# Performance work log

Measured on AMD Instinct MI355X. Metric: run time of the kernel, lower is better.

## Reference

```python
import jax, jax.numpy as jnp
from jax import lax
import numpy as np

RATIO = 4
CNT = 2  # sz=5 -> sz//2 in fineshift
B, C, H, W = 4, 8, 1024, 1024
K = 9

# --- half-pixel interpolation kernels (precomputed exactly as in fineshift) ---
_HALF = np.asarray([0.5, 0.305334091185, 0, -0.072698593239, 0, 0.021809577942,
                    0, -0.005192756653, 0, 0.000807762146, 0, -6.0081482e-05]) * 2.0
_FULL23 = np.concatenate([_HALF[1:][::-1], _HALF])   # 23-tap symmetric interp kernel
_DEC12 = _FULL23[::2]                                 # kernel[..., ::2] decimation -> 12 taps
K_S = np.concatenate([_DEC12, [0.0]])[:, None]        # 'S': (13,1), zero row appended
K_E = np.concatenate([_DEC12, [0.0]])[None, :]        # 'E': (1,13), zero col appended
K_SE = np.zeros((13, 13))
K_SE[:12, :12] = np.outer(_DEC12, _DEC12)             # 'SE': separable xy kernel + zero row/col


def _depthwise_same(x, k2d):
    # depthwise conv, identical kernel per band, torch padding='same' semantics
    c = x.shape[1]
    kh, kw = k2d.shape
    k = jnp.broadcast_to(jnp.asarray(k2d, x.dtype), (c, 1, kh, kw))
    pad = ((kh // 2, kh - 1 - kh // 2), (kw // 2, kw - 1 - kw // 2))
    return lax.conv_general_dilated(x, k, (1, 1), pad, feature_group_count=c)


def setup_inputs() -> dict:
    key = jax.random.key(0)
    k1, k2, k3, k4 = jax.random.split(key, 4)
    outputs = jax.random.normal(k1, (B, C, H, W), jnp.float32)
    mtf = jax.random.normal(k2, (K, K, C), jnp.float32) * 0.1
    r = jax.random.randint(k3, (B, C), 0, 5, jnp.int32)
    c = jax.random.randint(k4, (B, C), 0, 5, jnp.int32)
    return {"outputs": outputs, "mtf": mtf, "r": r, "c": c}


def reference(outputs, mtf, r, c):
    nb = outputs.shape[1]
    ksz = mtf.shape[0]
    pad = (ksz - 1) // 2
    # ReplicationPad2d + valid depthwise MTF blur (== pad + conv in original)
    xp = jnp.pad(outputs, ((0, 0), (0, 0), (pad, pad), (pad, pad)), mode='edge')
    w = jnp.transpose(mtf, (2, 0, 1))[:, None].astype(outputs.dtype)  # (C,1,K,K)
    x = lax.conv_general_dilated(xp, w, (1, 1), 'VALID', feature_group_count=nb)

    # --- fineshift, vectorized over batch and band (replaces per-batch loop + boolean masks) ---
    r_int, c_int = r // 2, c // 2
    r_frac, c_frac = r % 2, c % 2
    x_S = _depthwise_same(x, K_S)
    x_E = _depthwise_same(x, K_E)
    x_SE = _depthwise_same(x, K_SE)
    m = lambda cond: cond[:, :, None, None]
    x = jnp.where(m((r_frac == 1) & (c_frac == 1)), x_SE,
        jnp.where(m((r_frac == 1) & (c_frac == 0)), x_S,
        jnp.where(m((r_frac == 0) & (c_frac == 1)), x_E, x)))

    # integer shift: one-hot 5x5 'same' conv == out[y,x] = img[y - r_int, x - c_int], zeros outside
    hh, ww = x.shape[-2], x.shape[-1]
    def shift_one(img, ri, ci):
        p = jnp.pad(img, CNT)
        return lax.dynamic_slice(p, (CNT - ri, CNT - ci), (hh, ww))
    x = jax.vmap(jax.vmap(shift_one))(x, r_int, c_int)

    if RATIO == 2:
        return x[:, :, 1::RATIO, 1::RATIO]
    return x[:, :, 2::RATIO, 2::RATIO]
```

## Files before the change

kernel.cpp:

```cpp
#include <hip/hip_runtime.h>

typedef _Float16 half2v __attribute__((ext_vector_type(2)));
typedef _Float16 half4v __attribute__((ext_vector_type(4)));
typedef _Float16 half8v __attribute__((ext_vector_type(8)));

#define HH 1024
#define OHW 256
#define TH 16
#define TW 32
#define NR 80
#define NCH 18
#define ROWH 160
#define NTHREADS 256
#define ESPAN 528

#define NMAIN 4096
#define NEDGE 384
#define NCORN 288
#define NAUX  (NEDGE + NCORN)

#if defined(__has_builtin)
#  if __has_builtin(__builtin_amdgcn_fdot2)
#    define HAS_FDOT2 1
#  endif
#endif
#ifndef HAS_FDOT2
#  define HAS_FDOT2 0
#endif

__constant__ float DEC12c[12] = {
  -1.20162964e-04f,  1.615524292e-03f, -1.0385513306e-02f,  4.3619155884e-02f,
  -1.45397186478e-01f, 6.10668182370e-01f, 6.10668182370e-01f, -1.45397186478e-01f,
   4.3619155884e-02f, -1.0385513306e-02f,  1.615524292e-03f, -1.20162964e-04f
};

__device__ __forceinline__ int clampi(int v) { return v < 0 ? 0 : (v > HH - 1 ? HH - 1 : v); }

__device__ __forceinline__ int swzc(int c, int r) {
  return c ^ ((c >> 3) & 1) ^ ((r >> 2) & 3);
}

__device__ __forceinline__ half2v mk2(_Float16 a, _Float16 b) {
  half2v r; r.x = a; r.y = b; return r;
}

template<int J>
__device__ __forceinline__ half2v sel3(half8v a, half8v b, half8v c) {
  constexpr int V = J >> 2, E = J & 3;
  const half8v s = (V == 0) ? a : (V == 1) ? b : c;
  return mk2(s[2 * E], s[2 * E + 1]);
}
template<int E>
__device__ __forceinline__ half2v g2(half8v v) { return mk2(v[2 * E], v[2 * E + 1]); }

__device__ __forceinline__ float dot2acc(half2v w, half2v k, float acc) {
#if HAS_FDOT2
  return __builtin_amdgcn_fdot2(w, k, acc, false);
#else
  return acc + (float)w.x * (float)k.x + (float)w.y * (float)k.y;
#endif
}

__global__ __launch_bounds__(128) void dgp_ckbuild(
    const float* __restrict__ mtfp, const int* __restrict__ rp,
    const int* __restrict__ cp, _Float16* __restrict__ ckg) {
  __shared__ float kva[180];
  __shared__ float mlds[81];
  __shared__ float avs[12], bvs[12];
  const int tid = threadIdx.x;
  const int bz = blockIdx.x;
  const int chC = bz & 7;
  const int rv = rp[bz], cv = cp[bz];
  const int rf = rv & 1, cf = cv & 1;

  if (tid < 12)       avs[tid] = rf ? DEC12c[tid] : (tid == 6 ? 1.f : 0.f);
  else if (tid < 24)  bvs[tid - 12] = cf ? DEC12c[tid - 12] : (tid - 12 == 6 ? 1.f : 0.f);
  else if (tid < 105) { const int m = tid - 24; mlds[m] = mtfp[m * 8 + chC]; }
  __syncthreads();

  for (int i = tid; i < 180; i += 128) {
    const int S = i / 9, v = i - S * 9;
    const int plo = (S - 8 > 0) ? S - 8 : 0, phi = (S < 11) ? S : 11;
    float s1 = 0.f;
    for (int p = plo; p <= phi; ++p) s1 += avs[p] * mlds[(S - p) * 9 + v];
    kva[i] = s1;
  }
  __syncthreads();

  half2v* out2 = (half2v*)ckg;
  for (int i = tid; i < 200; i += 128) {
    const int S = i / 10, m = i - S * 10;
    float s[2];
    #pragma unroll
    for (int h = 0; h < 2; ++h) {
      const int T = 2 * m + h;
      const int qlo = (T - 8 > 0) ? T - 8 : 0, qhi = (T < 11) ? T : 11;
      float acc = 0.f;
      for (int q = qlo; q <= qhi; ++q) acc += bvs[q] * kva[S * 9 + (T - q)];
      s[h] = acc;
    }
    out2[bz * 320 + S * 16 + m] = mk2((_Float16)s[0], (_Float16)s[1]);
  }
}

__global__ __launch_bounds__(NTHREADS) void dgp_fused(
    const float* __restrict__ inp, const float* __restrict__ mtfp,
    const int* __restrict__ rp, const int* __restrict__ cp,
    const _Float16* __restrict__ ckg, float* __restrict__ outg,
    float* __restrict__ dumpf) {
  __shared__ __align__(64) unsigned char smem[25600];
  const int tid = threadIdx.x;
  const int b = blockIdx.x;

  if (b >= NAUX) {
    _Float16* tile = (_Float16*)smem;
    const int bm = b - NAUX;
    const int bxt = bm & 7, by = (bm >> 3) & 15, bz = bm >> 7;
    const int rv = rp[bz], cv = cp[bz];
    const int ri = rv >> 1, ci = cv >> 1;
    const int R0 = 4 * TH * by - 8 - ri;
    const int C0 = 4 * TW * bxt - 8 - ci;

    const float* src = inp + ((size_t)bz << 20);
    for (int idx = tid; idx < NR * NCH; idx += NTHREADS) {
      const int rr = idx / 18, g = idx - 18 * rr;
      const float* grow = src + (clampi(R0 + rr) << 10);
      const int c0 = C0 + 8 * g;
      float v[8];
      if (c0 >= 0 && c0 + 7 <= HH - 1) {
        __builtin_memcpy(v, grow + c0, 32);
      } else {
        #pragma unroll
        for (int i = 0; i < 8; ++i) v[i] = grow[clampi(c0 + i)];
      }
      _Float16 h[8];
      #pragma unroll
      for (int i = 0; i < 8; ++i) h[i] = (_Float16)v[i];
      __builtin_memcpy(tile + rr * ROWH + (swzc(g, rr) << 3), h, 16);
    }
    __syncthreads();

    const int ty = tid >> 4;
    const int tx = tid & 15;
    const int rbase = 4 * ty;
    const size_t kbase = (size_t)bz * 640;

    float a0e = 0.f, a0o = 0.f, a1e = 0.f, a1o = 0.f;

#define DOT_STEP(s_) do {                                                \
    const int r_ = rbase + (s_);                                         \
    const _Float16* rp_ = tile + r_ * ROWH;                              \
    const half8v w0 = *(const half8v*)(rp_ + (swzc(tx + 0, r_) << 3));   \
    const half8v w1 = *(const half8v*)(rp_ + (swzc(tx + 1, r_) << 3));   \
    const half8v w2 = *(const half8v*)(rp_ + (swzc(tx + 2, r_) << 3));   \
    const _Float16* kp_ = ckg + kbase + (s_) * 32;                       \
    const half8v K0 = *(const half8v*)(kp_);                             \
    const half8v K1 = *(const half8v*)(kp_ + 8);                         \
    const half4v K2 = *(const half4v*)(kp_ + 16);                        \
    a0e = dot2acc(sel3<0>(w0, w1, w2), g2<0>(K0), a0e);                  \
    a0o = dot2acc(sel3<1>(w0, w1, w2), g2<1>(K0), a0o);                  \
    a0e = dot2acc(sel3<2>(w0, w1, w2), g2<2>(K0), a0e);                  \
    a0o = dot2acc(sel3<3>(w0, w1, w2), g2<3>(K0), a0o);                  \
    a0e = dot2acc(sel3<4>(w0, w1, w2), g2<0>(K1), a0e);                  \
    a0o = dot2acc(sel3<5>(w0, w1, w2), g2<1>(K1), a0o);                  \
    a0e = dot2acc(sel3<6>(w0, w1, w2), g2<2>(K1), a0e);                  \
    a0o = dot2acc(sel3<7>(w0, w1, w2), g2<3>(K1), a0o);                  \
    a0e = dot2acc(sel3<8>(w0, w1, w2), mk2(K2[0], K2[1]), a0e);          \
    a0o = dot2acc(sel3<9>(w0, w1, w2), mk2(K2[2], K2[3]), a0o);          \
    a1e = dot2acc(sel3<2>(w0, w1, w2), g2<0>(K0), a1e);                  \
    a1o = dot2acc(sel3<3>(w0, w1, w2), g2<1>(K0), a1o);                  \
    a1e = dot2acc(sel3<4>(w0, w1, w2), g2<2>(K0), a1e);                  \
    a1o = dot2acc(sel3<5>(w0, w1, w2), g2<3>(K0), a1o);                  \
    a1e = dot2acc(sel3<6>(w0, w1, w2), g2<0>(K1), a1e);                  \
    a1o = dot2acc(sel3<7>(w0, w1, w2), g2<1>(K1), a1o);                  \
    a1e = dot2acc(sel3<8>(w0, w1, w2), g2<2>(K1), a1e);                  \
    a1o = dot2acc(sel3<9>(w0, w1, w2), g2<3>(K1), a1o);                  \
    a1e = dot2acc(sel3<10>(w0, w1, w2), mk2(K2[0], K2[1]), a1e);         \
    a1o = dot2acc(sel3<11>(w0, w1, w2), mk2(K2[2], K2[3]), a1o);         \
  } while (0)

    DOT_STEP(0);  DOT_STEP(1);  DOT_STEP(2);  DOT_STEP(3);  DOT_STEP(4);
    DOT_STEP(5);  DOT_STEP(6);  DOT_STEP(7);  DOT_STEP(8);  DOT_STEP(9);
    DOT_STEP(10); DOT_STEP(11); DOT_STEP(12); DOT_STEP(13); DOT_STEP(14);
    DOT_STEP(15); DOT_STEP(16); DOT_STEP(17); DOT_STEP(18); DOT_STEP(19);
#undef DOT_STEP

    const int oi = TH * by + ty;
    const int oj0 = TW * bxt + 2 * tx;
    const int oj1 = oj0 + 1;
    float* orow = outg + ((size_t)bz * OHW + oi) * OHW + oj0;
    float* dump = dumpf + tid;
    const bool rowbad = (oi < 2) | (oi == 255);
    float* d0 = (rowbad | (oj0 < 2) | (oj0 == 255)) ? dump : orow;
    float* d1 = (rowbad | (oj1 < 2) | (oj1 == 255)) ? dump : (orow + 1);
    *d0 = a0e + a0o;
    *d1 = a1e + a1o;
  } else if (b < NEDGE) {
    _Float16* tileh = (_Float16*)smem;
    float* ck   = (float*)(smem + 21120);
    float* kva  = (float*)(smem + 22720);
    float* mlds = (float*)(smem + 23440);
    float* avs  = (float*)(smem + 23764);
    float* bvs  = (float*)(smem + 23812);

    const int e = b;
    const int bx = e & 1;
    const int t = e >> 1;
    const int segi6 = t % 6;
    const int bz = t / 6;
    const bool isRow = (segi6 < 3);
    const int segi = isRow ? segi6 : segi6 - 3;
    const int fixedo = (segi == 2) ? 255 : segi;
    const int chC = bz & 7;
    const int rv = rp[bz], cv = cp[bz];
    const int ri = rv >> 1, rf = rv & 1, ci = cv >> 1, cf = cv & 1;

    if (tid < 12) {
      float av = rf ? DEC12c[tid] : (tid == 6 ? 1.f : 0.f);
      if (isRow) {
        const int xi = (2 + 4 * fixedo - ri) - 6 + tid;
        if (xi < 0 || xi >= HH) av = 0.f;
      }
      avs[tid] = av;
    } else if (tid < 24) {
      const int q = tid - 12;
      float bv = cf ? DEC12c[q] : (q == 6 ? 1.f : 0.f);
      if (!isRow) {
        const int xj = (2 + 4 * fixedo - ci) - 6 + q;
        if (xj < 0 || xj >= HH) bv = 0.f;
      }
      bvs[q] = bv;
    } else if (tid < 105) {
      const int m = tid - 24; mlds[m] = mtfp[m * 8 + chC];
    }
    __syncthreads();

    for (int i = tid; i < 180; i += NTHREADS) {
      const int S = i / 9, v = i - S * 9;
      const int plo = (S - 8 > 0) ? S - 8 : 0, phi = (S < 11) ? S : 11;
      float s1 = 0.f;
      for (int p = plo; p <= phi; ++p) s1 += avs[p] * mlds[(S - p) * 9 + v];
      kva[i] = s1;
    }
    __syncthreads();
    for (int i = tid; i < 400; i += NTHREADS) {
      const int S = i / 20, T = i - S * 20;
      const int qlo = (T - 8 > 0) ? T - 8 : 0, qhi = (T < 11) ? T : 11;
      float s1 = 0.f;
      for (int q = qlo; q <= qhi; ++q) s1 += bvs[q] * kva[S * 9 + (T - q)];
      ck[i] = s1;
    }

    const float* src = inp + ((size_t)bz << 20);
    if (isRow) {
      const int R0e = (2 + 4 * fixedo - ri) - 10;
      const int C0c = 512 * bx - 8 - ci;
      for (int i = tid; i < 20 * 66; i += NTHREADS) {
        const int rr = i / 66, jc = i - rr * 66;
        const float* grow = src + (clampi(R0e + rr) << 10);
        const int c0 = C0c + 8 * jc;
        float v[8];
        if (c0 >= 0 && c0 + 7 <= HH - 1) {
          __builtin_memcpy(v, grow + c0, 32);
        } else {
          #pragma unroll
          for (int k = 0; k < 8; ++k) v[k] = grow[clampi(c0 + k)];
        }
        _Float16 h[8];
        #pragma unroll
        for (int k = 0; k < 8; ++k) h[k] = (_Float16)v[k];
        __builtin_memcpy(tileh + rr * ESPAN + 8 * jc, h, 16);
      }
    } else {
      const int Cw0 = (2 + 4 * fixedo - ci) - 10;
      const int Rr0 = 512 * bx - 8 - ri;
      for (int i = tid; i < 20 * ESPAN; i += NTHREADS) {
        const int rr = i / 20, T = i - rr * 20;
        tileh[T * ESPAN + rr] =
            (_Float16)src[(clampi(Rr0 + rr) << 10) + clampi(Cw0 + T)];
      }
    }
    __syncthreads();

    if (tid < 128) {
      float acc = 0.f;
      for (int L = 0; L < 20; ++L) {
        const _Float16* wp = tileh + L * ESPAN + 4 * tid;
        #pragma unroll
        for (int j = 0; j < 5; ++j) {
          half4v h4;
          __builtin_memcpy(&h4, wp + 4 * j, 8);
          #pragma unroll
          for (int k = 0; k < 4; ++k) {
            const int ee = 4 * j + k;
            const float cv2 = isRow ? ck[L * 20 + ee] : ck[ee * 20 + L];
            acc += cv2 * (float)h4[k];
          }
        }
      }
      int oi, oj;
      if (isRow) { oi = fixedo; oj = 128 * bx + tid; }
      else       { oj = fixedo; oi = 128 * bx + tid; }
      const int ov = isRow ? oj : oi;
      if (ov != 0 && ov != 1 && ov != 255)
        outg[((size_t)bz * OHW + oi) * OHW + oj] = acc;
    }
  } else {
    float* mlds = (float*)smem;
    float* avs  = (float*)(smem + 324);
    float* bvs  = (float*)(smem + 372);

    const int c = b - NEDGE;
    const int bi = c % 3;
    const int t = c / 3;
    const int bj = t % 3;
    const int bz = t / 3;
    const int oi = (bi == 2) ? 255 : bi;
    const int oj = (bj == 2) ? 255 : bj;
    const int chC = bz & 7;
    const int rv = rp[bz], cv = cp[bz];
    const int ri = rv >> 1, rf = rv & 1, ci = cv >> 1, cf = cv & 1;

    if (tid < 12)       avs[tid] = rf ? DEC12c[tid] : (tid == 6 ? 1.f : 0.f);
    else if (tid < 24)  bvs[tid - 12] = cf ? DEC12c[tid - 12] : (tid - 12 == 6 ? 1.f : 0.f);
    if (tid < 81) mlds[tid] = mtfp[tid * 8 + chC];
    __syncthreads();
    if (tid >= 64) return;

    const int Ri = 2 + 4 * oi - ri;
    const int Cj = 2 + 4 * oj - ci;
    const float* src = inp + ((size_t)bz << 20);

    float acc = 0.f;
    for (int pair = tid; pair < 144; pair += 64) {
      const int p = pair / 12, q = pair - 12 * (pair / 12);
      const int xi = Ri - 6 + p, xj = Cj - 6 + q;
      if (xi < 0 || xi >= HH || xj < 0 || xj >= HH) continue;
      const float ab = avs[p] * bvs[q];
      if (ab == 0.f) continue;
      float s = 0.f;
      #pragma unroll
      for (int u = 0; u < 9; ++u) {
        const float* grow = src + (clampi(xi - 4 + u) << 10);
        #pragma unroll
        for (int v = 0; v < 9; ++v) s += mlds[u * 9 + v] * grow[clampi(xj - 4 + v)];
      }
      acc += ab * s;
    }
    #pragma unroll
    for (int off = 32; off > 0; off >>= 1) acc += __shfl_down(acc, off);
    if (tid == 0) outg[((size_t)bz * OHW + oi) * OHW + oj] = acc;
  }
}

extern "C" void kernel_launch(void* const* d_in, const int* in_sizes, int n_in,
                              void* d_out, int out_size, void* d_ws, size_t ws_size,
                              hipStream_t stream) {
  const float* inp  = (const float*)d_in[0];
  const float* mtfp = (const float*)d_in[1];
  const int*   rp   = (const int*)d_in[2];
  const int*   cp   = (const int*)d_in[3];
  float* outg = (float*)d_out;
  _Float16* ckg = (_Float16*)d_ws;
  float* dumpf = (float*)((char*)d_ws + 49152);

  hipLaunchKernelGGL(dgp_ckbuild, dim3(32), dim3(128), 0, stream, mtfp, rp, cp, ckg);
  hipLaunchKernelGGL(dgp_fused, dim3(NMAIN + NAUX), dim3(NTHREADS), 0, stream,
                     inp, mtfp, rp, cp, (const _Float16*)ckg, outg, dumpf);
}
```

Before: 91.20 us.

## Compute four outputs per thread with doubled tile width in main conv blocks

Each thread of the main blocks now computes four adjacent output columns instead of two. The shared tile width doubles to 64 output columns and the main block count halves. This reuses each staged input vector across more outputs and amortises the constant-kernel loads and the tile halo over more work, cutting LDS reads and global halo traffic per output. In exchange it raises shared memory to about 45 KB and adds accumulators and registers, which can reduce occupancy, and the grid has fewer blocks.

```diff
diff --git a/kernel.cpp b/kernel.cpp
--- a/kernel.cpp
+++ b/kernel.cpp
@@ -7,14 +7,14 @@
 #define HH 1024
 #define OHW 256
 #define TH 16
-#define TW 32
+#define TW 64
 #define NR 80
-#define NCH 18
-#define ROWH 160
+#define NCH 34
+#define ROWH 288
 #define NTHREADS 256
 #define ESPAN 528
 
-#define NMAIN 4096
+#define NMAIN 2048
 #define NEDGE 384
 #define NCORN 288
 #define NAUX  (NEDGE + NCORN)
@@ -45,9 +45,9 @@
 }
 
 template<int J>
-__device__ __forceinline__ half2v sel3(half8v a, half8v b, half8v c) {
+__device__ __forceinline__ half2v sel4(half8v a, half8v b, half8v c, half8v d) {
   constexpr int V = J >> 2, E = J & 3;
-  const half8v s = (V == 0) ? a : (V == 1) ? b : c;
+  const half8v s = (V == 0) ? a : (V == 1) ? b : (V == 2) ? c : d;
   return mk2(s[2 * E], s[2 * E + 1]);
 }
 template<int E>
@@ -108,14 +108,14 @@
     const int* __restrict__ rp, const int* __restrict__ cp,
     const _Float16* __restrict__ ckg, float* __restrict__ outg,
     float* __restrict__ dumpf) {
-  __shared__ __align__(64) unsigned char smem[25600];
+  __shared__ __align__(64) unsigned char smem[46080];
   const int tid = threadIdx.x;
   const int b = blockIdx.x;
 
   if (b >= NAUX) {
     _Float16* tile = (_Float16*)smem;
     const int bm = b - NAUX;
-    const int bxt = bm & 7, by = (bm >> 3) & 15, bz = bm >> 7;
+    const int bxt = bm & 3, by = (bm >> 2) & 15, bz = bm >> 6;
     const int rv = rp[bz], cv = cp[bz];
     const int ri = rv >> 1, ci = cv >> 1;
     const int R0 = 4 * TH * by - 8 - ri;
@@ -123,7 +123,7 @@
 
     const float* src = inp + ((size_t)bz << 20);
     for (int idx = tid; idx < NR * NCH; idx += NTHREADS) {
-      const int rr = idx / 18, g = idx - 18 * rr;
+      const int rr = idx / 34, g = idx - 34 * rr;
       const float* grow = src + (clampi(R0 + rr) << 10);
       const int c0 = C0 + 8 * g;
       float v[8];
@@ -145,38 +145,36 @@
     const int rbase = 4 * ty;
     const size_t kbase = (size_t)bz * 640;
 
-    float a0e = 0.f, a0o = 0.f, a1e = 0.f, a1o = 0.f;
+    float s0e = 0.f, s0o = 0.f, s1e = 0.f, s1o = 0.f;
+    float s2e = 0.f, s2o = 0.f, s3e = 0.f, s3o = 0.f;
+
+#define OUTM(m, Ae, Ao, w0, w1, w2, w3, K0, K1, K2)                      \
+    Ae = dot2acc(sel4<2*(m) + 0>(w0, w1, w2, w3), g2<0>(K0), Ae);        \
+    Ao = dot2acc(sel4<2*(m) + 1>(w0, w1, w2, w3), g2<1>(K0), Ao);        \
+    Ae = dot2acc(sel4<2*(m) + 2>(w0, w1, w2, w3), g2<2>(K0), Ae);        \
+    Ao = dot2acc(sel4<2*(m) + 3>(w0, w1, w2, w3), g2<3>(K0), Ao);        \
+    Ae = dot2acc(sel4<2*(m) + 4>(w0, w1, w2, w3), g2<0>(K1), Ae);        \
+    Ao = dot2acc(sel4<2*(m) + 5>(w0, w1, w2, w3), g2<1>(K1), Ao);        \
+    Ae = dot2acc(sel4<2*(m) + 6>(w0, w1, w2, w3), g2<2>(K1), Ae);        \
+    Ao = dot2acc(sel4<2*(m) + 7>(w0, w1, w2, w3), g2<3>(K1), Ao);        \
+    Ae = dot2acc(sel4<2*(m) + 8>(w0, w1, w2, w3), mk2(K2[0], K2[1]), Ae);\
+    Ao = dot2acc(sel4<2*(m) + 9>(w0, w1, w2, w3), mk2(K2[2], K2[3]), Ao);
 
 #define DOT_STEP(s_) do {                                                \
     const int r_ = rbase + (s_);                                         \
     const _Float16* rp_ = tile + r_ * ROWH;                              \
-    const half8v w0 = *(const half8v*)(rp_ + (swzc(tx + 0, r_) << 3));   \
-    const half8v w1 = *(const half8v*)(rp_ + (swzc(tx + 1, r_) << 3));   \
-    const half8v w2 = *(const half8v*)(rp_ + (swzc(tx + 2, r_) << 3));   \
+    const half8v w0 = *(const half8v*)(rp_ + (swzc(2 * tx + 0, r_) << 3)); \
+    const half8v w1 = *(const half8v*)(rp_ + (swzc(2 * tx + 1, r_) << 3)); \
+    const half8v w2 = *(const half8v*)(rp_ + (swzc(2 * tx + 2, r_) << 3)); \
+    const half8v w3 = *(const half8v*)(rp_ + (swzc(2 * tx + 3, r_) << 3)); \
     const _Float16* kp_ = ckg + kbase + (s_) * 32;                       \
     const half8v K0 = *(const half8v*)(kp_);                             \
     const half8v K1 = *(const half8v*)(kp_ + 8);                         \
     const half4v K2 = *(const half4v*)(kp_ + 16);                        \
-    a0e = dot2acc(sel3<0>(w0, w1, w2), g2<0>(K0), a0e);                  \
-    a0o = dot2acc(sel3<1>(w0, w1, w2), g2<1>(K0), a0o);                  \
-    a0e = dot2acc(sel3<2>(w0, w1, w2), g2<2>(K0), a0e);                  \
-    a0o = dot2acc(sel3<3>(w0, w1, w2), g2<3>(K0), a0o);                  \
-    a0e = dot2acc(sel3<4>(w0, w1, w2), g2<0>(K1), a0e);                  \
-    a0o = dot2acc(sel3<5>(w0, w1, w2), g2<1>(K1), a0o);                  \
-    a0e = dot2acc(sel3<6>(w0, w1, w2), g2<2>(K1), a0e);                  \
-    a0o = dot2acc(sel3<7>(w0, w1, w2), g2<3>(K1), a0o);                  \
-    a0e = dot2acc(sel3<8>(w0, w1, w2), mk2(K2[0], K2[1]), a0e);          \
-    a0o = dot2acc(sel3<9>(w0, w1, w2), mk2(K2[2], K2[3]), a0o);          \
-    a1e = dot2acc(sel3<2>(w0, w1, w2), g2<0>(K0), a1e);                  \
-    a1o = dot2acc(sel3<3>(w0, w1, w2), g2<1>(K0), a1o);                  \
-    a1e = dot2acc(sel3<4>(w0, w1, w2), g2<2>(K0), a1e);                  \
-    a1o = dot2acc(sel3<5>(w0, w1, w2), g2<3>(K0), a1o);                  \
-    a1e = dot2acc(sel3<6>(w0, w1, w2), g2<0>(K1), a1e);                  \
-    a1o = dot2acc(sel3<7>(w0, w1, w2), g2<1>(K1), a1o);                  \
-    a1e = dot2acc(sel3<8>(w0, w1, w2), g2<2>(K1), a1e);                  \
-    a1o = dot2acc(sel3<9>(w0, w1, w2), g2<3>(K1), a1o);                  \
-    a1e = dot2acc(sel3<10>(w0, w1, w2), mk2(K2[0], K2[1]), a1e);         \
-    a1o = dot2acc(sel3<11>(w0, w1, w2), mk2(K2[2], K2[3]), a1o);         \
+    OUTM(0, s0e, s0o, w0, w1, w2, w3, K0, K1, K2)                        \
+    OUTM(1, s1e, s1o, w0, w1, w2, w3, K0, K1, K2)                        \
+    OUTM(2, s2e, s2o, w0, w1, w2, w3, K0, K1, K2)                        \
+    OUTM(3, s3e, s3o, w0, w1, w2, w3, K0, K1, K2)                        \
   } while (0)
 
     DOT_STEP(0);  DOT_STEP(1);  DOT_STEP(2);  DOT_STEP(3);  DOT_STEP(4);
@@ -184,17 +182,21 @@
     DOT_STEP(10); DOT_STEP(11); DOT_STEP(12); DOT_STEP(13); DOT_STEP(14);
     DOT_STEP(15); DOT_STEP(16); DOT_STEP(17); DOT_STEP(18); DOT_STEP(19);
 #undef DOT_STEP
+#undef OUTM
 
     const int oi = TH * by + ty;
-    const int oj0 = TW * bxt + 2 * tx;
-    const int oj1 = oj0 + 1;
+    const int oj0 = TW * bxt + 4 * tx;
     float* orow = outg + ((size_t)bz * OHW + oi) * OHW + oj0;
     float* dump = dumpf + tid;
     const bool rowbad = (oi < 2) | (oi == 255);
-    float* d0 = (rowbad | (oj0 < 2) | (oj0 == 255)) ? dump : orow;
-    float* d1 = (rowbad | (oj1 < 2) | (oj1 == 255)) ? dump : (orow + 1);
-    *d0 = a0e + a0o;
-    *d1 = a1e + a1o;
+    float* d0 = (rowbad | (oj0 + 0 < 2) | (oj0 + 0 == 255)) ? dump : (orow + 0);
+    float* d1 = (rowbad | (oj0 + 1 < 2) | (oj0 + 1 == 255)) ? dump : (orow + 1);
+    float* d2 = (rowbad | (oj0 + 2 < 2) | (oj0 + 2 == 255)) ? dump : (orow + 2);
+    float* d3 = (rowbad | (oj0 + 3 < 2) | (oj0 + 3 == 255)) ? dump : (orow + 3);
+    *d0 = s0e + s0o;
+    *d1 = s1e + s1o;
+    *d2 = s2e + s2o;
+    *d3 = s3e + s3o;
   } else if (b < NEDGE) {
     _Float16* tileh = (_Float16*)smem;
     float* ck   = (float*)(smem + 21120);
```

Result: slower. 108.9 us (+19.4%).
